# Kernel optimization log

Hardware: AMD Instinct MI355X
Metric: run time of the kernel (lower is better)

The kernel has to match this reference:

```python
import jax, jax.numpy as jnp
import numpy as np

P, RES_H, RES_W = 32, 256, 256
H, W = 480, 640
FOCAL = 1.0


def setup_inputs() -> dict:
    key = jax.random.key(0)
    k1, k2, k3, k4 = jax.random.split(key, 4)
    # texture: alpha + rgb logits, uniform(-1,1) as in torch init
    plane_content = jax.random.uniform(k1, (P, 4, RES_H, RES_W), jnp.float32, -1.0, 1.0)
    # orthonormal plane basis (columns = plane x/y axes + normal)
    plane_basis, _ = jnp.linalg.qr(jax.random.normal(k2, (P, 3, 3), jnp.float32))
    xy = jax.random.normal(k3, (P, 2), jnp.float32)
    z = 2.0 + 4.0 * jax.random.uniform(k4, (P, 1), jnp.float32)  # planes in front of camera
    plane_position = jnp.concatenate([xy, z], axis=-1)
    plane_wh = jnp.full((P, 2), 2.0, jnp.float32)
    cam_R = jnp.eye(3, dtype=jnp.float32)   # world-to-cam rotation
    cam_T = jnp.zeros((3,), jnp.float32)    # world-to-cam translation
    return {"plane_content": plane_content, "plane_basis": plane_basis,
            "plane_position": plane_position, "plane_wh": plane_wh,
            "cam_R": cam_R, "cam_T": cam_T}


def _bilinear(img, uv):
    # img: (C, Hc, Wc); uv: (N, 2) in [-1, 1]. torch grid_sample bilinear,
    # align_corners=False, padding_mode='zeros'.
    C, Hc, Wc = img.shape
    x = (uv[:, 0] + 1.0) * Wc * 0.5 - 0.5
    y = (uv[:, 1] + 1.0) * Hc * 0.5 - 0.5
    x0 = jnp.floor(x)
    y0 = jnp.floor(y)
    wx = x - x0
    wy = y - y0

    def gather(xi, yi):
        inb = (xi >= 0) & (xi < Wc) & (yi >= 0) & (yi < Hc)
        xc = jnp.clip(xi, 0, Wc - 1).astype(jnp.int32)
        yc = jnp.clip(yi, 0, Hc - 1).astype(jnp.int32)
        return jnp.where(inb[None, :], img[:, yc, xc], 0.0)  # (C, N)

    v00 = gather(x0, y0)
    v01 = gather(x0 + 1.0, y0)
    v10 = gather(x0, y0 + 1.0)
    v11 = gather(x0 + 1.0, y0 + 1.0)
    top = v00 * (1.0 - wx) + v01 * wx
    bot = v10 * (1.0 - wx) + v11 * wx
    return (top * (1.0 - wy) + bot * wy).T  # (N, C)


def reference(plane_content, plane_basis, plane_position, plane_wh, cam_R, cam_T):
    N = H * W
    xs = ((jnp.arange(W, dtype=jnp.float32) + 0.5) / W) * 2.0 - 1.0
    ys = ((jnp.arange(H, dtype=jnp.float32) + 0.5) / H) * 2.0 - 1.0
    gy, gx = jnp.meshgrid(ys, xs, indexing='ij')
    # pinhole ray directions in camera frame (z-depth parameterization)
    dirs_cam = jnp.stack([gx.reshape(-1) / FOCAL, gy.reshape(-1) / FOCAL,
                          jnp.ones((N,), jnp.float32)], axis=-1)  # (N,3)
    cam_pos = -cam_R.T @ cam_T                 # camera center in world
    dirs_world = dirs_cam @ cam_R              # R^T d per ray, (N,3)

    normals = plane_basis[:, :, 2]             # (P,3)
    num = jnp.einsum('pc,pc->p', normals, plane_position - cam_pos[None])
    den = jnp.einsum('pc,nc->pn', normals, dirs_world)
    den = jnp.where(jnp.abs(den) < 1e-6, 1e-6, den)
    points_depth = num[:, None] / den          # (P,N) depth on each plane

    world_points = cam_pos[None, None] + points_depth[..., None] * dirs_world[None]  # (P,N,3)
    local = jnp.einsum('pnc,pcd->pnd', world_points - plane_position[:, None], plane_basis)
    uv = local[..., :2] / (plane_wh[:, None, :] * 0.5)        # normalize to [-1,1] inside plane
    in_planes = jnp.all(jnp.abs(uv) <= 1.0, axis=-1)          # (P,N)

    raw = jax.vmap(_bilinear)(plane_content, uv)              # (P,N,4)
    content = jnp.where(in_planes[..., None], jax.nn.sigmoid(raw), 0.0)

    sort_idx = jnp.argsort(points_depth, axis=0)              # front-to-back per pixel
    depth_sorted = jnp.take_along_axis(points_depth, sort_idx, axis=0)
    content_sorted = jnp.take_along_axis(content, sort_idx[..., None], axis=0)

    alpha = content_sorted[..., 0]                            # (P,N)
    color = content_sorted[..., 1:]                           # (P,N,3)
    trans = jnp.cumprod(1.0 - alpha, axis=0)
    trans = jnp.concatenate([jnp.ones((1, N), alpha.dtype), trans[:-1]], axis=0)
    weight = alpha * trans                                    # (P,N)

    depth_img = jnp.sum(depth_sorted * weight, axis=0).reshape(H, W)
    color_img = jnp.sum(color * weight[..., None], axis=0).reshape(H, W, 3)
    return jnp.concatenate([color_img, depth_img[..., None]], axis=-1)  # (H,W,4)
```

## Files before the change

kernel.cpp:

```cpp
#include <hip/hip_runtime.h>
#include <cstdint>

constexpr int P   = 32;
constexpr int RES = 256;
constexpr int H   = 480;
constexpr int W   = 640;
#define KMAX 0xFFFFFFFFu

__device__ __forceinline__ uint32_t mono_key(float f) {
    uint32_t b = __float_as_uint(f);
    return (b & 0x80000000u) ? ~b : (b | 0x80000000u);
}
__device__ __forceinline__ float unmono(uint32_t m) {
    uint32_t b = (m & 0x80000000u) ? (m ^ 0x80000000u) : ~m;
    return __uint_as_float(b);
}
__device__ __forceinline__ float h2f(unsigned short u) {
    return (float)__builtin_bit_cast(_Float16, u);
}
__device__ __forceinline__ unsigned short f2h(float f) {
    return __builtin_bit_cast(unsigned short, (_Float16)f);
}

__global__ __launch_bounds__(256) void prep_repack_kernel(
    const float* __restrict__ content,
    const float* __restrict__ basis, const float* __restrict__ ppos,
    const float* __restrict__ pwh,   const float* __restrict__ camR,
    const float* __restrict__ camT,
    float4* __restrict__ tab, ushort4* __restrict__ tex)
{
    const int tid = blockIdx.x * 256 + threadIdx.x;
    const float* src = content + (((size_t)(tid >> 16)) << 18) + (tid & 65535);
    ushort4 o;
    o.x = f2h(src[0]);
    o.y = f2h(src[65536]);
    o.z = f2h(src[131072]);
    o.w = f2h(src[196608]);
    tex[tid] = o;

    if (blockIdx.x == 0 && threadIdx.x < P) {
        const int p = threadIdx.x;
        const float T0=camT[0],T1=camT[1],T2=camT[2];
        const float cpx = -(camR[0]*T0 + camR[3]*T1 + camR[6]*T2);
        const float cpy = -(camR[1]*T0 + camR[4]*T1 + camR[7]*T2);
        const float cpz = -(camR[2]*T0 + camR[5]*T1 + camR[8]*T2);
        const float* b = basis + 9 * p;
        const float n0 = b[2], n1 = b[5], n2 = b[8];
        const float px = ppos[3*p], py = ppos[3*p+1], pz = ppos[3*p+2];
        const float num = n0*(px-cpx) + n1*(py-cpy) + n2*(pz-cpz);
        const float A0  = (cpx-px)*b[0] + (cpy-py)*b[3] + (cpz-pz)*b[6];
        const float A1  = (cpx-px)*b[1] + (cpy-py)*b[4] + (cpz-pz)*b[7];
        const float hw0 = pwh[2*p]   * 0.5f;
        const float hw1 = pwh[2*p+1] * 0.5f;
        tab[4*p+0] = make_float4(n0, n1, n2, num);
        tab[4*p+1] = make_float4(A0, A1, __int_as_float(p << 16), 0.f);
        tab[4*p+2] = make_float4(b[0], b[3], b[6], 1.0f/hw0);
        tab[4*p+3] = make_float4(b[1], b[4], b[7], 1.0f/hw1);
    }
}

__global__ __launch_bounds__(128) void render_fast(
    const ushort4* __restrict__ tex, const float4* __restrict__ tab,
    const float* __restrict__ camR,  float* __restrict__ out)
{
    __shared__ float4   s_pl[P][3];
    __shared__ uint32_t s_key[2][16][64];
    __shared__ uint2    s_c4 [2][16][64];

    const int t    = threadIdx.x;
    const int lane = t & 63;
    const int w    = t >> 6;

    if (t < P) {
        s_pl[t][0] = tab[4*t+1];
        s_pl[t][1] = tab[4*t+2];
        s_pl[t][2] = tab[4*t+3];
    }
    #pragma unroll
    for (int e = 0; e < 16; ++e) s_key[w][e][lane] = KMAX;
    __syncthreads();

    const int x = blockIdx.x * 16 + (lane & 15);
    const int y = blockIdx.y * 4  + (lane >> 4);
    const float gx = ((float)x + 0.5f) / (float)W * 2.0f - 1.0f;
    const float gy = ((float)y + 0.5f) / (float)H * 2.0f - 1.0f;
    const float dwx = gx*camR[0] + gy*camR[3] + camR[6];
    const float dwy = gx*camR[1] + gy*camR[4] + camR[7];
    const float dwz = gx*camR[2] + gy*camR[5] + camR[8];

    const int pb = __builtin_amdgcn_readfirstlane(w) * 16;

    uint32_t key[16];
    #pragma unroll
    for (int p = 0; p < 16; ++p) {
        const float4 c0 = tab[4*(pb+p)+0];
        const float4 c1 = tab[4*(pb+p)+1];
        const float4 c2 = tab[4*(pb+p)+2];
        const float4 c3 = tab[4*(pb+p)+3];
        float den = c0.x*dwx + c0.y*dwy + c0.z*dwz;
        if (fabsf(den) < 1e-6f) den = 1e-6f;
        const float d  = c0.w / den;
        const float B0 = c2.x*dwx + c2.y*dwy + c2.z*dwz;
        const float B1 = c3.x*dwx + c3.y*dwy + c3.z*dwz;
        const float u  = (c1.x + d*B0) * c2.w;
        const float v  = (c1.y + d*B1) * c3.w;
        key[p] = (fabsf(u) <= 1.0f && fabsf(v) <= 1.0f) ? mono_key(d) : KMAX;
    }

    auto argmin_pop = [&](int& obi) -> uint32_t {
        uint32_t bk = KMAX; int bi = 0;
        #pragma unroll
        for (int i = 0; i < 16; ++i) {
            const bool c = key[i] < bk;
            bk = c ? key[i] : bk;
            bi = c ? i : bi;
        }
        #pragma unroll
        for (int i = 0; i < 16; ++i)
            key[i] = (i == bi) ? KMAX : key[i];
        obi = bi;
        return bk;
    };

    struct St { ushort4 t00, t01, t10, t11; float wx, wy; int ix, iy; uint32_t key; };

    auto issue = [&](uint32_t k, int bi) -> St {
        St s;
        s.key = k;
        const bool valid = (k != KMAX);
        const float d = valid ? unmono(k) : 0.0f;
        const int g = pb + bi;
        const float4 pA = s_pl[g][0];
        const float4 pB = s_pl[g][1];
        const float4 pC = s_pl[g][2];
        const float B0 = pB.x*dwx + pB.y*dwy + pB.z*dwz;
        const float B1 = pC.x*dwx + pC.y*dwy + pC.z*dwz;
        const float u  = (pA.x + d*B0) * pB.w;
        const float v  = (pA.y + d*B1) * pC.w;
        const float fx = (u + 1.0f) * 128.0f - 0.5f;
        const float fy = (v + 1.0f) * 128.0f - 0.5f;
        const float x0f = floorf(fx), y0f = floorf(fy);
        s.wx = fx - x0f; s.wy = fy - y0f;
        s.ix = (int)x0f; s.iy = (int)y0f;
        const int x0c = min(max(s.ix,     0), RES-1);
        const int x1c = min(max(s.ix + 1, 0), RES-1);
        const int y0c = min(max(s.iy,     0), RES-1);
        const int y1c = min(max(s.iy + 1, 0), RES-1);
        const int base = __float_as_int(pA.z);
        const int r0 = base + (y0c << 8), r1 = base + (y1c << 8);
        s.t00 = tex[r0 + x0c]; s.t01 = tex[r0 + x1c];
        s.t10 = tex[r1 + x0c]; s.t11 = tex[r1 + x1c];
        return s;
    };

    auto store = [&](const St& s, int e) {
        if (s.key == KMAX) return;
        ushort4 t00 = s.t00, t01 = s.t01, t10 = s.t10, t11 = s.t11;
        const bool mx0 = (uint32_t)s.ix       < (uint32_t)RES;
        const bool mx1 = (uint32_t)(s.ix + 1) < (uint32_t)RES;
        const bool my0 = (uint32_t)s.iy       < (uint32_t)RES;
        const bool my1 = (uint32_t)(s.iy + 1) < (uint32_t)RES;
        if (!(mx0 && my0)) { t00.x = t00.y = t00.z = t00.w = 0; }
        if (!(mx1 && my0)) { t01.x = t01.y = t01.z = t01.w = 0; }
        if (!(mx0 && my1)) { t10.x = t10.y = t10.z = t10.w = 0; }
        if (!(mx1 && my1)) { t11.x = t11.y = t11.z = t11.w = 0; }
        const float omwx = 1.0f - s.wx, omwy = 1.0f - s.wy;
        const unsigned short* q00 = (const unsigned short*)&t00;
        const unsigned short* q01 = (const unsigned short*)&t01;
        const unsigned short* q10 = (const unsigned short*)&t10;
        const unsigned short* q11 = (const unsigned short*)&t11;
        float c4[4];
        #pragma unroll
        for (int c = 0; c < 4; ++c) {
            const float top = h2f(q00[c]) * omwx + h2f(q01[c]) * s.wx;
            const float bot = h2f(q10[c]) * omwx + h2f(q11[c]) * s.wx;
            const float raw = top * omwy + bot * s.wy;
            c4[c] = __builtin_amdgcn_rcpf(1.0f + __expf(-raw));
        }
        s_key[w][e][lane] = s.key;
        s_c4[w][e][lane]  = make_uint2(
            (uint32_t)f2h(c4[0]) | ((uint32_t)f2h(c4[1]) << 16),
            (uint32_t)f2h(c4[2]) | ((uint32_t)f2h(c4[3]) << 16));
    };

    int e = 0;
    int cbi; uint32_t ck = argmin_pop(cbi);
    if (__ballot(ck != KMAX) != 0ull) {
        St cur = issue(ck, cbi);
        for (;;) {
            int nbi; const uint32_t nk = argmin_pop(nbi);
            const bool more = (__ballot(nk != KMAX) != 0ull);
            St nxt;
            if (more) nxt = issue(nk, nbi);
            store(cur, e); ++e;
            if (!more) break;
            cur = nxt;
        }
    }
    __syncthreads();

    const int q  = w * 32 + (t & 31);
    const bool act = (t & 63) < 32;
    int i0 = 0, i1 = 0;
    uint32_t k0 = act ? s_key[0][0][q] : KMAX;
    uint32_t k1 = act ? s_key[1][0][q] : KMAX;
    float aR = 0.f, aG = 0.f, aB = 0.f, aD = 0.f, tr = 1.f;

    while (__ballot(k0 != KMAX || k1 != KMAX) != 0ull) {
        const bool take0 = (k0 <= k1);
        const uint32_t k = take0 ? k0 : k1;
        const bool valid = (k != KMAX);
        const int  li = (take0 ? i0 : i1) & 15;
        const uint2 cp = s_c4[take0 ? 0 : 1][li][q];
        if (take0) { ++i0; k0 = (i0 < 16) ? s_key[0][i0][q] : KMAX; }
        else       { ++i1; k1 = (i1 < 16) ? s_key[1][i1][q] : KMAX; }
        const float a  = valid ? h2f((unsigned short)(cp.x & 0xFFFFu)) : 0.0f;
        const float cR = valid ? h2f((unsigned short)(cp.x >> 16))     : 0.0f;
        const float cG = valid ? h2f((unsigned short)(cp.y & 0xFFFFu)) : 0.0f;
        const float cB = valid ? h2f((unsigned short)(cp.y >> 16))     : 0.0f;
        const float d  = valid ? unmono(k) : 0.0f;
        const float wgt = a * tr;
        aD += d  * wgt;
        aR += cR * wgt;
        aG += cG * wgt;
        aB += cB * wgt;
        tr *= (1.0f - a);
    }

    if (act) {
        const int px = blockIdx.x * 16 + (q & 15);
        const int py = blockIdx.y * 4  + (q >> 4);
        float4 res; res.x = aR; res.y = aG; res.z = aB; res.w = aD;
        *reinterpret_cast<float4*>(out + (py * W + px) * 4) = res;
    }
}

__global__ __launch_bounds__(256) void render_ref(
    const float* __restrict__ content, const float* __restrict__ basis,
    const float* __restrict__ ppos,    const float* __restrict__ pwh,
    const float* __restrict__ camR,    const float* __restrict__ camT,
    float* __restrict__ out)
{
    __shared__ float s_pl[P][20];
    const int t = threadIdx.x;
    const int x = blockIdx.x * 16 + (t & 15);
    const int y = blockIdx.y * 16 + (t >> 4);
    if (t < P) {
        const float* b = basis + t * 9;
        s_pl[t][0] = b[0]; s_pl[t][1] = b[3]; s_pl[t][2] = b[6];
        s_pl[t][3] = b[1]; s_pl[t][4] = b[4]; s_pl[t][5] = b[7];
        s_pl[t][6] = ppos[t*3+0]; s_pl[t][7] = ppos[t*3+1]; s_pl[t][8] = ppos[t*3+2];
        s_pl[t][9] = pwh[t*2+0] * 0.5f; s_pl[t][10] = pwh[t*2+1] * 0.5f;
    }
    __syncthreads();
    const float T0=camT[0],T1=camT[1],T2=camT[2];
    const float cpx = -(camR[0]*T0 + camR[3]*T1 + camR[6]*T2);
    const float cpy = -(camR[1]*T0 + camR[4]*T1 + camR[7]*T2);
    const float cpz = -(camR[2]*T0 + camR[5]*T1 + camR[8]*T2);
    const float gx = ((float)x + 0.5f) / (float)W * 2.0f - 1.0f;
    const float gy = ((float)y + 0.5f) / (float)H * 2.0f - 1.0f;
    const float dwx = gx*camR[0] + gy*camR[3] + camR[6];
    const float dwy = gx*camR[1] + gy*camR[4] + camR[7];
    const float dwz = gx*camR[2] + gy*camR[5] + camR[8];
    uint32_t key[P];
    #pragma unroll
    for (int p = 0; p < P; ++p) {
        const float b00=basis[p*9+0], b01=basis[p*9+1], n0=basis[p*9+2];
        const float b10=basis[p*9+3], b11=basis[p*9+4], n1=basis[p*9+5];
        const float b20=basis[p*9+6], b21=basis[p*9+7], n2=basis[p*9+8];
        const float px=ppos[p*3+0], py=ppos[p*3+1], pz=ppos[p*3+2];
        const float hw0=pwh[p*2+0]*0.5f, hw1=pwh[p*2+1]*0.5f;
        const float num = n0*(px-cpx) + n1*(py-cpy) + n2*(pz-cpz);
        float den = n0*dwx + n1*dwy + n2*dwz;
        if (fabsf(den) < 1e-6f) den = 1e-6f;
        const float depth = num / den;
        const float ox = cpx + depth*dwx - px;
        const float oy = cpy + depth*dwy - py;
        const float oz = cpz + depth*dwz - pz;
        const float u = (ox*b00 + oy*b10 + oz*b20) / hw0;
        const float v = (ox*b01 + oy*b11 + oz*b21) / hw1;
        key[p] = (fabsf(u) <= 1.0f && fabsf(v) <= 1.0f) ? mono_key(depth) : KMAX;
    }
    float aR=0.f,aG=0.f,aB=0.f,aD=0.f,tr=1.f;
    #pragma unroll 1
    for (int it = 0; it < P; ++it) {
        uint32_t bk = KMAX; int bi = 0;
        #pragma unroll
        for (int i = 0; i < P; ++i) {
            const bool c = key[i] < bk;
            bk = c ? key[i] : bk; bi = c ? i : bi;
        }
        if (bk == KMAX) break;
        #pragma unroll
        for (int i = 0; i < P; ++i) key[i] = (i == bi) ? KMAX : key[i];
        const float depth = unmono(bk);
        const float* pl = s_pl[bi];
        const float ox = cpx + depth*dwx - pl[6];
        const float oy = cpy + depth*dwy - pl[7];
        const float oz = cpz + depth*dwz - pl[8];
        const float u = (ox*pl[0] + oy*pl[1] + oz*pl[2]) / pl[9];
        const float v = (ox*pl[3] + oy*pl[4] + oz*pl[5]) / pl[10];
        const float fx = (u + 1.0f) * 128.0f - 0.5f;
        const float fy = (v + 1.0f) * 128.0f - 0.5f;
        const float x0f = floorf(fx), y0f = floorf(fy);
        const float wx = fx - x0f, wy = fy - y0f;
        const int ix = (int)x0f, iy = (int)y0f;
        const int x0c = min(max(ix,0),RES-1), x1c = min(max(ix+1,0),RES-1);
        const int y0c = min(max(iy,0),RES-1), y1c = min(max(iy+1,0),RES-1);
        const float m00 = ((uint32_t)ix<(uint32_t)RES && (uint32_t)iy<(uint32_t)RES) ? 1.f:0.f;
        const float m01 = ((uint32_t)(ix+1)<(uint32_t)RES && (uint32_t)iy<(uint32_t)RES) ? 1.f:0.f;
        const float m10 = ((uint32_t)ix<(uint32_t)RES && (uint32_t)(iy+1)<(uint32_t)RES) ? 1.f:0.f;
        const float m11 = ((uint32_t)(ix+1)<(uint32_t)RES && (uint32_t)(iy+1)<(uint32_t)RES) ? 1.f:0.f;
        const int o00=y0c*RES+x0c, o01=y0c*RES+x1c, o10=y1c*RES+x0c, o11=y1c*RES+x1c;
        const float* pc = content + ((size_t)bi << 18);
        float c4[4];
        #pragma unroll
        for (int c = 0; c < 4; ++c) {
            const float* ic = pc + (c << 16);
            const float v00 = ic[o00]*m00, v01 = ic[o01]*m01;
            const float v10 = ic[o10]*m10, v11 = ic[o11]*m11;
            const float top = v00*(1.f-wx) + v01*wx;
            const float bot = v10*(1.f-wx) + v11*wx;
            const float raw = top*(1.f-wy) + bot*wy;
            c4[c] = 1.0f / (1.0f + __expf(-raw));
        }
        const float wgt = c4[0]*tr;
        aD += depth*wgt; aR += c4[1]*wgt; aG += c4[2]*wgt; aB += c4[3]*wgt;
        tr *= (1.0f - c4[0]);
    }
    const int o = (y * W + x) * 4;
    float4 res; res.x=aR; res.y=aG; res.z=aB; res.w=aD;
    *reinterpret_cast<float4*>(out + o) = res;
}

extern "C" void kernel_launch(void* const* d_in, const int* in_sizes, int n_in,
                              void* d_out, int out_size, void* d_ws, size_t ws_size,
                              hipStream_t stream) {
    const float* content = (const float*)d_in[0];
    const float* basis   = (const float*)d_in[1];
    const float* ppos    = (const float*)d_in[2];
    const float* pwh     = (const float*)d_in[3];
    const float* camR    = (const float*)d_in[4];
    const float* camT    = (const float*)d_in[5];

    const size_t TAB_BYTES = 2048;
    const size_t need = TAB_BYTES + (size_t)P * 65536 * sizeof(ushort4);

    if (ws_size >= need) {
        float4*  tab = (float4*)d_ws;
        ushort4* tex = (ushort4*)((char*)d_ws + TAB_BYTES);
        prep_repack_kernel<<<P * 65536 / 256, 256, 0, stream>>>(
            content, basis, ppos, pwh, camR, camT, tab, tex);
        render_fast<<<dim3(W / 16, H / 4), dim3(128), 0, stream>>>(
            tex, tab, camR, (float*)d_out);
    } else {
        dim3 grid(W / 16, H / 16);
        render_ref<<<grid, dim3(256), 0, stream>>>(
            content, basis, ppos, pwh, camR, camT, (float*)d_out);
    }
}
```

Measured before the change: 35.65 us.

## Store fp16 texture in 4x4 tiled layout with vectorized repack

The repack kernel now writes the packed fp16 RGBA texture in 4x4 texel tiles instead of row-major order. Each thread converts a whole tile using float4 loads, and the launch uses 16x fewer threads. The render kernel's bilinear fetches use a matching tiled address function, so the four neighbouring texels more often fall in the same cache lines. The costs are extra address arithmetic per fetch, and the repack now has fewer threads issuing strided 16-byte writes.

```diff
diff --git a/kernel.cpp b/kernel.cpp
--- a/kernel.cpp
+++ b/kernel.cpp
@@ -20,6 +20,10 @@
 }
 __device__ __forceinline__ unsigned short f2h(float f) {
     return __builtin_bit_cast(unsigned short, (_Float16)f);
+}
+
+__device__ __forceinline__ int tex_addr(int base, int xx, int yy) {
+    return base + ((((yy >> 2) << 6) | (xx >> 2)) << 4) + ((yy & 3) << 2) + (xx & 3);
 }
 
 __global__ __launch_bounds__(256) void prep_repack_kernel(
@@ -30,32 +34,48 @@
     float4* __restrict__ tab, ushort4* __restrict__ tex)
 {
     const int tid = blockIdx.x * 256 + threadIdx.x;
-    const float* src = content + (((size_t)(tid >> 16)) << 18) + (tid & 65535);
-    ushort4 o;
-    o.x = f2h(src[0]);
-    o.y = f2h(src[65536]);
-    o.z = f2h(src[131072]);
-    o.w = f2h(src[196608]);
-    tex[tid] = o;
+    const int p   = tid >> 12;
+    const int blk = tid & 4095;
+    const int by  = blk >> 6, bx = blk & 63;
+    const float* src = content + ((size_t)p << 18);
+    ushort4* dst = tex + ((size_t)tid << 4);
+
+    #pragma unroll
+    for (int dy = 0; dy < 4; ++dy) {
+        const int ti = ((by << 2) + dy) * 256 + (bx << 2);
+        const float4 c0 = *reinterpret_cast<const float4*>(src + ti);
+        const float4 c1 = *reinterpret_cast<const float4*>(src + 65536  + ti);
+        const float4 c2 = *reinterpret_cast<const float4*>(src + 131072 + ti);
+        const float4 c3 = *reinterpret_cast<const float4*>(src + 196608 + ti);
+        ushort4 o;
+        o.x = f2h(c0.x); o.y = f2h(c1.x); o.z = f2h(c2.x); o.w = f2h(c3.x);
+        dst[(dy << 2) + 0] = o;
+        o.x = f2h(c0.y); o.y = f2h(c1.y); o.z = f2h(c2.y); o.w = f2h(c3.y);
+        dst[(dy << 2) + 1] = o;
+        o.x = f2h(c0.z); o.y = f2h(c1.z); o.z = f2h(c2.z); o.w = f2h(c3.z);
+        dst[(dy << 2) + 2] = o;
+        o.x = f2h(c0.w); o.y = f2h(c1.w); o.z = f2h(c2.w); o.w = f2h(c3.w);
+        dst[(dy << 2) + 3] = o;
+    }
 
     if (blockIdx.x == 0 && threadIdx.x < P) {
-        const int p = threadIdx.x;
+        const int q = threadIdx.x;
         const float T0=camT[0],T1=camT[1],T2=camT[2];
         const float cpx = -(camR[0]*T0 + camR[3]*T1 + camR[6]*T2);
         const float cpy = -(camR[1]*T0 + camR[4]*T1 + camR[7]*T2);
         const float cpz = -(camR[2]*T0 + camR[5]*T1 + camR[8]*T2);
-        const float* b = basis + 9 * p;
+        const float* b = basis + 9 * q;
         const float n0 = b[2], n1 = b[5], n2 = b[8];
-        const float px = ppos[3*p], py = ppos[3*p+1], pz = ppos[3*p+2];
+        const float px = ppos[3*q], py = ppos[3*q+1], pz = ppos[3*q+2];
         const float num = n0*(px-cpx) + n1*(py-cpy) + n2*(pz-cpz);
         const float A0  = (cpx-px)*b[0] + (cpy-py)*b[3] + (cpz-pz)*b[6];
         const float A1  = (cpx-px)*b[1] + (cpy-py)*b[4] + (cpz-pz)*b[7];
-        const float hw0 = pwh[2*p]   * 0.5f;
-        const float hw1 = pwh[2*p+1] * 0.5f;
-        tab[4*p+0] = make_float4(n0, n1, n2, num);
-        tab[4*p+1] = make_float4(A0, A1, __int_as_float(p << 16), 0.f);
-        tab[4*p+2] = make_float4(b[0], b[3], b[6], 1.0f/hw0);
-        tab[4*p+3] = make_float4(b[1], b[4], b[7], 1.0f/hw1);
+        const float hw0 = pwh[2*q]   * 0.5f;
+        const float hw1 = pwh[2*q+1] * 0.5f;
+        tab[4*q+0] = make_float4(n0, n1, n2, num);
+        tab[4*q+1] = make_float4(A0, A1, __int_as_float(q << 16), 0.f);
+        tab[4*q+2] = make_float4(b[0], b[3], b[6], 1.0f/hw0);
+        tab[4*q+3] = make_float4(b[1], b[4], b[7], 1.0f/hw1);
     }
 }
 
@@ -147,9 +167,10 @@
         const int y0c = min(max(s.iy,     0), RES-1);
         const int y1c = min(max(s.iy + 1, 0), RES-1);
         const int base = __float_as_int(pA.z);
-        const int r0 = base + (y0c << 8), r1 = base + (y1c << 8);
-        s.t00 = tex[r0 + x0c]; s.t01 = tex[r0 + x1c];
-        s.t10 = tex[r1 + x0c]; s.t11 = tex[r1 + x1c];
+        s.t00 = tex[tex_addr(base, x0c, y0c)];
+        s.t01 = tex[tex_addr(base, x1c, y0c)];
+        s.t10 = tex[tex_addr(base, x0c, y1c)];
+        s.t11 = tex[tex_addr(base, x1c, y1c)];
         return s;
     };
 
@@ -349,7 +370,7 @@
     if (ws_size >= need) {
         float4*  tab = (float4*)d_ws;
         ushort4* tex = (ushort4*)((char*)d_ws + TAB_BYTES);
-        prep_repack_kernel<<<P * 65536 / 256, 256, 0, stream>>>(
+        prep_repack_kernel<<<P * 4096 / 256, 256, 0, stream>>>(
             content, basis, ppos, pwh, camR, camT, tab, tex);
         render_fast<<<dim3(W / 16, H / 4), dim3(128), 0, stream>>>(
             tex, tab, camR, (float*)d_out);
```

Result: slower. 38.75 us (+8.7%).
